# Performance work log

Hardware: AMD Instinct MI355X
Metric: run time of the kernel (lower is better)

## Reference

```python
import jax, jax.numpy as jnp
import numpy as np

B, C, H, W = 4, 128, 64, 64


def setup_inputs() -> dict:
    key = jax.random.key(0)
    ks = jax.random.split(key, 7)
    s = 1.0 / np.sqrt(C)
    return {
        "x": jax.random.normal(ks[0], (B, C, H, W), dtype=jnp.float32),
        "Wq": jax.random.normal(ks[1], (C, C), dtype=jnp.float32) * s,
        "bq": jnp.zeros((C,), dtype=jnp.float32),
        "Wk": jax.random.normal(ks[2], (C, C), dtype=jnp.float32) * s,
        "bk": jnp.zeros((C,), dtype=jnp.float32),
        "Wv": jax.random.normal(ks[3], (C, C), dtype=jnp.float32) * s,
        "bv": jnp.zeros((C,), dtype=jnp.float32),
    }


def reference(x, Wq, bq, Wk, bk, Wv, bv):
    b, c, h, w = x.shape
    n = h * w
    scale = c ** (-0.5)
    # tokens: [B, N, C]
    xt = x.reshape(b, c, n).transpose(0, 2, 1)
    # 1x1 convs == per-token channel GEMMs (out[c'] = sum_c W[c',c] x[c] + b[c'])
    q = jnp.einsum("bnc,dc->bnd", xt, Wq) + bq  # [B, N, C]
    k = jnp.einsum("bnc,dc->bnd", xt, Wk) + bk  # [B, N, C]
    v = jnp.einsum("bnc,dc->bnd", xt, Wv) + bv  # [B, N, C]
    scores = jnp.einsum("bic,bjc->bij", q, k) * scale  # [B, N, N]
    attn = jax.nn.softmax(scores, axis=-1)
    out = jnp.einsum("bij,bjc->bic", attn, v)  # [B, N, C]
    return out.transpose(0, 2, 1).reshape(b, c, h, w)
```

## Files before the change

kernel.cpp:

```cpp
#include <hip/hip_runtime.h>
#include <hip/hip_bf16.h>


#define BATCH 4
#define CH    128
#define NTOK  4096
#define SCALE 0.08838834764831845f
#define LOG2E 1.4426950408889634f
#define MFIX  16.0f

typedef __attribute__((ext_vector_type(8)))  short short8;
typedef __attribute__((ext_vector_type(4)))  float f32x4;
typedef __attribute__((ext_vector_type(16))) float f32x16;

static __device__ __forceinline__ unsigned short f2bf(float f) {
    __hip_bfloat16 h = (__hip_bfloat16)f;
    return *(const unsigned short*)&h;
}

static __device__ __forceinline__ unsigned cvt_pk_bf16(float lo, float hi) {
    unsigned r;
    asm("v_cvt_pk_bf16_f32 %0, %1, %2" : "=v"(r) : "v"(lo), "v"(hi));
    return r;
}

static __device__ __forceinline__ short8 pack_bf16x8(float4 a, float4 b) {
    union { unsigned u[4]; short8 s8; } f;
    f.u[0] = cvt_pk_bf16(a.x, a.y);
    f.u[1] = cvt_pk_bf16(a.z, a.w);
    f.u[2] = cvt_pk_bf16(b.x, b.y);
    f.u[3] = cvt_pk_bf16(b.z, b.w);
    return f.s8;
}

__global__ __launch_bounds__(256) void proj_mfma_kernel(
    const float* __restrict__ x,
    const float* __restrict__ Wq, const float* __restrict__ Wk,
    const float* __restrict__ Wv,
    const float* __restrict__ bq, const float* __restrict__ bk,
    const float* __restrict__ bv,
    unsigned short* __restrict__ q_ws, unsigned short* __restrict__ kf_ws,
    unsigned short* __restrict__ vf_ws)
{
    __shared__ __align__(16) unsigned short Wl[CH * CH];
    __shared__ __align__(16) unsigned short XsT[64 * CH];

    const int t    = threadIdx.x;
    const int w    = t >> 6;
    const int lane = t & 63;
    const int quad = lane >> 4;
    const int c16  = lane & 15;
    const int n0   = blockIdx.x * 64;
    const int b    = blockIdx.y;
    const int z    = blockIdx.z;
    const float* xb = x + (size_t)b * CH * NTOK;
    const float* wm = (z == 0) ? Wq : (z == 1) ? Wk : Wv;

    #pragma unroll
    for (int i = 0; i < 8; ++i) {
        const int f   = i * 256 + t;
        const int row = f >> 4;
        const int u   = f & 15;
        const float* src = wm + f * 8;
        const float4 a = *(const float4*)src;
        const float4 c = *(const float4*)(src + 4);
        *(short8*)&Wl[row * CH + ((u ^ (row & 15)) << 3)] = pack_bf16x8(a, c);
    }
    {
        const int tok = lane;
        #pragma unroll
        for (int cc = 0; cc < 4; ++cc) {
            const int cb = 32 * w + 8 * cc;
            float xv[8];
            #pragma unroll
            for (int j = 0; j < 8; ++j)
                xv[j] = xb[(size_t)(cb + j) * NTOK + n0 + tok];
            union { unsigned u[4]; short8 s8; } pk;
            #pragma unroll
            for (int j = 0; j < 4; ++j)
                pk.u[j] = cvt_pk_bf16(xv[2 * j], xv[2 * j + 1]);
            const int phys = ((cb >> 3) ^ (tok & 15));
            *(short8*)&XsT[tok * CH + phys * 8] = pk.s8;
        }
    }
    __syncthreads();

    if (z < 2) {
        const float* bias = (z == 0) ? bq : bk;
        const float mul = (z == 0) ? (SCALE * LOG2E) : 1.0f;
        short8 xa[4];
        #pragma unroll
        for (int ks = 0; ks < 4; ++ks)
            xa[ks] = *(const short8*)&XsT[(16 * w + c16) * CH + (((4 * ks + quad) ^ c16) << 3)];
        #pragma unroll
        for (int nt = 0; nt < 8; ++nt) {
            f32x4 a = (f32x4){0.f, 0.f, 0.f, 0.f};
            #pragma unroll
            for (int ks = 0; ks < 4; ++ks) {
                const short8 bf = *(const short8*)
                    &Wl[(16 * nt + c16) * CH + (((4 * ks + quad) ^ c16) << 3)];
                a = __builtin_amdgcn_mfma_f32_16x16x32_bf16(xa[ks], bf, a, 0, 0, 0);
            }
            const float bvv = bias[16 * nt + c16];
            #pragma unroll
            for (int r = 0; r < 4; ++r) {
                const int n = n0 + 16 * w + quad * 4 + r;
                if (z == 0) {
                    q_ws[((size_t)b * NTOK + n) * CH + 16 * nt + c16] =
                        f2bf((a[r] + bvv) * mul);
                } else {
                    const size_t idx =
                        (((size_t)b * (NTOK >> 5) + (n >> 5)) * 8 + nt) * 512
                        + ((n & 31) + 32 * (c16 >> 3)) * 8 + (c16 & 7);
                    kf_ws[idx] = f2bf(a[r] + bvv);
                }
            }
        }
    } else {
        #pragma unroll
        for (int nt = 0; nt < 4; ++nt) {
            short8 xbf[4];
            #pragma unroll
            for (int ks = 0; ks < 4; ++ks)
                xbf[ks] = *(const short8*)&XsT[(16 * nt + c16) * CH + (((4 * ks + quad) ^ c16) << 3)];
            #pragma unroll
            for (int mt = 0; mt < 2; ++mt) {
                const int crow16 = 16 * (2 * w + mt);
                f32x4 acc = (f32x4){0.f, 0.f, 0.f, 0.f};
                #pragma unroll
                for (int ks = 0; ks < 4; ++ks) {
                    const short8 wva = *(const short8*)
                        &Wl[(crow16 + c16) * CH + (((4 * ks + quad) ^ c16) << 3)];
                    acc = __builtin_amdgcn_mfma_f32_16x16x32_bf16(wva, xbf[ks], acc, 0, 0, 0);
                }
                #pragma unroll
                for (int r = 0; r < 4; ++r) {
                    const int ch  = crow16 + quad * 4 + r;
                    const int tok = n0 + 16 * nt + c16;
                    const size_t idx =
                        ((((size_t)b * (NTOK >> 5) + (tok >> 5)) * 2
                          + ((tok >> 4) & 1)) * 4 + (ch >> 5)) * 512
                        + ((ch & 31) + 32 * ((tok >> 3) & 1)) * 8 + (tok & 7);
                    vf_ws[idx] = f2bf(acc[r] + bv[ch]);
                }
            }
        }
    }
}

template <int SPLIT>
__global__ __launch_bounds__(256, 2) void flash_attn_mfma(
    const unsigned short* __restrict__ q_ws,
    const unsigned short* __restrict__ kf_ws,
    const unsigned short* __restrict__ vf_ws,
    float* __restrict__ out,
    float* __restrict__ Op, float* __restrict__ l_p)
{
    const int t    = threadIdx.x;
    const int w    = t >> 6;
    const int lane = t & 63;
    const int half = lane >> 5;
    const int l32  = lane & 31;

    int xx, jc, b;
    if constexpr (SPLIT % 2 == 0) {
        const int bid = blockIdx.x;
        b = (bid & 7) >> 1;
        const int sub = (bid & 1) * (16 * SPLIT) + (bid >> 3);
        jc = sub >> 5;
        xx = sub & 31;
    } else {
        const int bid = blockIdx.x;
        xx = bid & 31;
        jc = 0;
        b  = bid >> 5;
    }

    const int n0   = xx * 128;
    const int jbeg = jc * (NTOK / SPLIT);
    constexpr int NT2 = (NTOK / SPLIT) / 32;

    const unsigned short* kg = kf_ws + (size_t)b * NTOK * CH;
    const unsigned short* vg = vf_ws + (size_t)b * NTOK * CH;

    short8 qa[8];
    {
        const unsigned short* qrow =
            q_ws + ((size_t)b * NTOK + n0 + 32 * w + l32) * CH;
        #pragma unroll
        for (int ks = 0; ks < 8; ++ks)
            qa[ks] = *(const short8*)(qrow + ks * 16 + half * 8);
    }

    f32x16 Oa[4];
    #pragma unroll
    for (int ct = 0; ct < 4; ++ct) Oa[ct] = (f32x16)(0.0f);
    float lsum = 0.f;

    short8 kf[8];
    auto KF_LOAD = [&](int jj) {
        const unsigned short* kb = kg + (size_t)(jj >> 5) * (8 * 512);
        #pragma unroll
        for (int ks = 0; ks < 8; ++ks)
            kf[ks] = *(const short8*)(kb + (ks * 64 + lane) * 8);
    };

    KF_LOAD(jbeg);

    for (int i = 0; i < w; ++i) __builtin_amdgcn_s_sleep(4);

    int j0 = jbeg;
    for (int tt = 0; tt < NT2; ++tt, j0 += 32) {
        f32x16 s = (f32x16)(-MFIX);
        __builtin_amdgcn_s_setprio(1);
        #pragma unroll
        for (int ks = 0; ks < 8; ++ks)
            s = __builtin_amdgcn_mfma_f32_32x32x16_bf16(kf[ks], qa[ks], s, 0, 0, 0);
        __builtin_amdgcn_s_setprio(0);

        short8 vfA[4], vfB[4];
        {
            const unsigned short* vb = vg + (size_t)(j0 >> 5) * (8 * 512);
            #pragma unroll
            for (int ct = 0; ct < 4; ++ct)
                vfA[ct] = *(const short8*)(vb + ((0 * 4 + ct) * 64 + lane) * 8);
            #pragma unroll
            for (int ct = 0; ct < 4; ++ct)
                vfB[ct] = *(const short8*)(vb + ((1 * 4 + ct) * 64 + lane) * 8);
        }
        if (tt + 1 < NT2) KF_LOAD(j0 + 32);

        float p[16];
        #pragma unroll
        for (int r = 0; r < 16; ++r) p[r] = exp2f(s[r]);
        {
            float a0 = 0.f, a1 = 0.f, a2 = 0.f, a3 = 0.f;
            #pragma unroll
            for (int r = 0; r < 4; ++r) {
                a0 += p[r]; a1 += p[4 + r]; a2 += p[8 + r]; a3 += p[12 + r];
            }
            lsum += (a0 + a1) + (a2 + a3);
        }
        short8 pb0, pb1;
        {
            unsigned wd[8];
            #pragma unroll
            for (int i = 0; i < 8; ++i) wd[i] = cvt_pk_bf16(p[2 * i], p[2 * i + 1]);
            auto r02 = __builtin_amdgcn_permlane32_swap(wd[0], wd[2], false, false);
            auto r13 = __builtin_amdgcn_permlane32_swap(wd[1], wd[3], false, false);
            auto r46 = __builtin_amdgcn_permlane32_swap(wd[4], wd[6], false, false);
            auto r57 = __builtin_amdgcn_permlane32_swap(wd[5], wd[7], false, false);
            union { unsigned u[4]; short8 s8; } f0, f1;
            f0.u[0] = r02[0]; f0.u[1] = r13[0]; f0.u[2] = r02[1]; f0.u[3] = r13[1];
            f1.u[0] = r46[0]; f1.u[1] = r57[0]; f1.u[2] = r46[1]; f1.u[3] = r57[1];
            pb0 = f0.s8;
            pb1 = f1.s8;
        }

        __builtin_amdgcn_s_setprio(1);
        #pragma unroll
        for (int ct = 0; ct < 4; ++ct)
            Oa[ct] = __builtin_amdgcn_mfma_f32_32x32x16_bf16(vfA[ct], pb0, Oa[ct], 0, 0, 0);
        #pragma unroll
        for (int ct = 0; ct < 4; ++ct)
            Oa[ct] = __builtin_amdgcn_mfma_f32_32x32x16_bf16(vfB[ct], pb1, Oa[ct], 0, 0, 0);
        __builtin_amdgcn_s_setprio(0);
    }

    const float lt = lsum + __shfl_xor(lsum, 32);
    const int n = n0 + 32 * w + l32;

    if constexpr (SPLIT == 1) {
        const float inv = 1.0f / lt;
        #pragma unroll
        for (int ct = 0; ct < 4; ++ct) {
            #pragma unroll
            for (int r = 0; r < 16; ++r) {
                const int c = 32 * ct + (r & 3) + 8 * (r >> 2) + 4 * half;
                out[((size_t)b * CH + c) * NTOK + n] = Oa[ct][r] * inv;
            }
        }
    } else {
        const size_t chunk = (size_t)(b * SPLIT + jc);
        #pragma unroll
        for (int ct = 0; ct < 4; ++ct) {
            #pragma unroll
            for (int r = 0; r < 16; ++r) {
                const int c = 32 * ct + (r & 3) + 8 * (r >> 2) + 4 * half;
                Op[(chunk * CH + c) * NTOK + n] = Oa[ct][r];
            }
        }
        if (half == 0) l_p[chunk * NTOK + n] = lt;
    }
}

template <int SPLIT>
__global__ __launch_bounds__(256) void combine_kernel(
    const float* __restrict__ Op, const float* __restrict__ l_p,
    float* __restrict__ out)
{
    const int b = blockIdx.y;
    const size_t idx = ((size_t)blockIdx.x * 256 + threadIdx.x) * 4;
    const int c = (int)(idx >> 12);
    const int n = (int)(idx & (NTOK - 1));
    float4 acc = make_float4(0.f, 0.f, 0.f, 0.f);
    float4 den = make_float4(0.f, 0.f, 0.f, 0.f);
    #pragma unroll
    for (int j = 0; j < SPLIT; ++j) {
        const size_t chunk = (size_t)(b * SPLIT + j);
        const float4 o = *(const float4*)&Op[(chunk * CH + c) * NTOK + n];
        const float4 d = *(const float4*)&l_p[chunk * NTOK + n];
        acc.x += o.x; acc.y += o.y; acc.z += o.z; acc.w += o.w;
        den.x += d.x; den.y += d.y; den.z += d.z; den.w += d.w;
    }
    float4 r;
    r.x = acc.x / den.x; r.y = acc.y / den.y;
    r.z = acc.z / den.z; r.w = acc.w / den.w;
    *(float4*)&out[((size_t)b * CH * NTOK) + idx] = r;
}

extern "C" void kernel_launch(void* const* d_in, const int* in_sizes, int n_in,
                              void* d_out, int out_size, void* d_ws, size_t ws_size,
                              hipStream_t stream) {
    const float* x  = (const float*)d_in[0];
    const float* Wq = (const float*)d_in[1];
    const float* bq = (const float*)d_in[2];
    const float* Wk = (const float*)d_in[3];
    const float* bk = (const float*)d_in[4];
    const float* Wv = (const float*)d_in[5];
    const float* bv = (const float*)d_in[6];
    float* out = (float*)d_out;

    const size_t QKV = (size_t)BATCH * NTOK * CH;
    unsigned short* q_ws  = (unsigned short*)d_ws;
    unsigned short* kf_ws = q_ws + QKV;
    unsigned short* vf_ws = kf_ws + QKV;
    float* Op = (float*)(vf_ws + QKV);

    const size_t baseBytes = 3 * QKV * 2;
    auto needBytes = [&](size_t S) {
        return baseBytes + S * BATCH * NTOK * (size_t)(CH * 4 + 4);
    };

    dim3 gp(NTOK / 64, BATCH, 3);
    proj_mfma_kernel<<<gp, 256, 0, stream>>>(x, Wq, Wk, Wv, bq, bk, bv,
                                             q_ws, kf_ws, vf_ws);

    dim3 gc(CH * NTOK / 1024, BATCH);
    if (ws_size >= needBytes(4)) {
        float* l_p = Op + (size_t)4 * BATCH * NTOK * CH;
        flash_attn_mfma<4><<<dim3(128 * 4), 256, 0, stream>>>(
            q_ws, kf_ws, vf_ws, out, Op, l_p);
        combine_kernel<4><<<gc, 256, 0, stream>>>(Op, l_p, out);
    } else {
        flash_attn_mfma<1><<<dim3(32 * BATCH), 256, 0, stream>>>(
            q_ws, kf_ws, vf_ws, out, nullptr, nullptr);
    }
}
```

Before: 127.2 us.

## Software-pipeline attention loop: overlap next tile's QK^T with current softmax

Restructures the attention inner loop so QK^T for tile t+1 is issued while the softmax of tile t is computed, with K and V loads prefetched one tile ahead. The aim is to hide exp and permute latency behind MFMA work and to keep the matrix unit busy. It also removes the per-wave s_sleep stagger and the s_setprio priority hints. In exchange it holds two score accumulators live at once, which raises register pressure and could lower occupancy.

```diff
diff --git a/kernel.cpp b/kernel.cpp
--- a/kernel.cpp
+++ b/kernel.cpp
@@ -179,6 +179,7 @@
     const int n0   = xx * 128;
     const int jbeg = jc * (NTOK / SPLIT);
     constexpr int NT2 = (NTOK / SPLIT) / 32;
+    static_assert(NT2 >= 2, "pipeline needs >= 2 tiles");
 
     const unsigned short* kg = kf_ws + (size_t)b * NTOK * CH;
     const unsigned short* vg = vf_ws + (size_t)b * NTOK * CH;
@@ -198,73 +199,82 @@
     float lsum = 0.f;
 
     short8 kf[8];
+    short8 vfA[4], vfB[4];
+
     auto KF_LOAD = [&](int jj) {
         const unsigned short* kb = kg + (size_t)(jj >> 5) * (8 * 512);
         #pragma unroll
         for (int ks = 0; ks < 8; ++ks)
             kf[ks] = *(const short8*)(kb + (ks * 64 + lane) * 8);
     };
-
-    KF_LOAD(jbeg);
-
-    for (int i = 0; i < w; ++i) __builtin_amdgcn_s_sleep(4);
-
-    int j0 = jbeg;
-    for (int tt = 0; tt < NT2; ++tt, j0 += 32) {
-        f32x16 s = (f32x16)(-MFIX);
-        __builtin_amdgcn_s_setprio(1);
+    auto VF_LOAD = [&](int jj) {
+        const unsigned short* vb = vg + (size_t)(jj >> 5) * (8 * 512);
+        #pragma unroll
+        for (int ct = 0; ct < 4; ++ct)
+            vfA[ct] = *(const short8*)(vb + ((0 * 4 + ct) * 64 + lane) * 8);
+        #pragma unroll
+        for (int ct = 0; ct < 4; ++ct)
+            vfB[ct] = *(const short8*)(vb + ((1 * 4 + ct) * 64 + lane) * 8);
+    };
+    auto QKT = [&](f32x16& s) {
         #pragma unroll
         for (int ks = 0; ks < 8; ++ks)
             s = __builtin_amdgcn_mfma_f32_32x32x16_bf16(kf[ks], qa[ks], s, 0, 0, 0);
-        __builtin_amdgcn_s_setprio(0);
-
-        short8 vfA[4], vfB[4];
-        {
-            const unsigned short* vb = vg + (size_t)(j0 >> 5) * (8 * 512);
-            #pragma unroll
-            for (int ct = 0; ct < 4; ++ct)
-                vfA[ct] = *(const short8*)(vb + ((0 * 4 + ct) * 64 + lane) * 8);
-            #pragma unroll
-            for (int ct = 0; ct < 4; ++ct)
-                vfB[ct] = *(const short8*)(vb + ((1 * 4 + ct) * 64 + lane) * 8);
-        }
-        if (tt + 1 < NT2) KF_LOAD(j0 + 32);
-
+    };
+    auto SOFTMAX = [&](const f32x16& s, short8& pb0, short8& pb1) {
         float p[16];
         #pragma unroll
         for (int r = 0; r < 16; ++r) p[r] = exp2f(s[r]);
-        {
-            float a0 = 0.f, a1 = 0.f, a2 = 0.f, a3 = 0.f;
-            #pragma unroll
-            for (int r = 0; r < 4; ++r) {
-                a0 += p[r]; a1 += p[4 + r]; a2 += p[8 + r]; a3 += p[12 + r];
-            }
-            lsum += (a0 + a1) + (a2 + a3);
-        }
-        short8 pb0, pb1;
-        {
-            unsigned wd[8];
-            #pragma unroll
-            for (int i = 0; i < 8; ++i) wd[i] = cvt_pk_bf16(p[2 * i], p[2 * i + 1]);
-            auto r02 = __builtin_amdgcn_permlane32_swap(wd[0], wd[2], false, false);
-            auto r13 = __builtin_amdgcn_permlane32_swap(wd[1], wd[3], false, false);
-            auto r46 = __builtin_amdgcn_permlane32_swap(wd[4], wd[6], false, false);
-            auto r57 = __builtin_amdgcn_permlane32_swap(wd[5], wd[7], false, false);
-            union { unsigned u[4]; short8 s8; } f0, f1;
-            f0.u[0] = r02[0]; f0.u[1] = r13[0]; f0.u[2] = r02[1]; f0.u[3] = r13[1];
-            f1.u[0] = r46[0]; f1.u[1] = r57[0]; f1.u[2] = r46[1]; f1.u[3] = r57[1];
-            pb0 = f0.s8;
-            pb1 = f1.s8;
-        }
-
-        __builtin_amdgcn_s_setprio(1);
+        float a0 = 0.f, a1 = 0.f, a2 = 0.f, a3 = 0.f;
+        #pragma unroll
+        for (int r = 0; r < 4; ++r) {
+            a0 += p[r]; a1 += p[4 + r]; a2 += p[8 + r]; a3 += p[12 + r];
+        }
+        lsum += (a0 + a1) + (a2 + a3);
+        unsigned wd[8];
+        #pragma unroll
+        for (int i = 0; i < 8; ++i) wd[i] = cvt_pk_bf16(p[2 * i], p[2 * i + 1]);
+        auto r02 = __builtin_amdgcn_permlane32_swap(wd[0], wd[2], false, false);
+        auto r13 = __builtin_amdgcn_permlane32_swap(wd[1], wd[3], false, false);
+        auto r46 = __builtin_amdgcn_permlane32_swap(wd[4], wd[6], false, false);
+        auto r57 = __builtin_amdgcn_permlane32_swap(wd[5], wd[7], false, false);
+        union { unsigned u[4]; short8 s8; } f0, f1;
+        f0.u[0] = r02[0]; f0.u[1] = r13[0]; f0.u[2] = r02[1]; f0.u[3] = r13[1];
+        f1.u[0] = r46[0]; f1.u[1] = r57[0]; f1.u[2] = r46[1]; f1.u[3] = r57[1];
+        pb0 = f0.s8;
+        pb1 = f1.s8;
+    };
+    auto PV = [&](const short8& pb0, const short8& pb1) {
         #pragma unroll
         for (int ct = 0; ct < 4; ++ct)
             Oa[ct] = __builtin_amdgcn_mfma_f32_32x32x16_bf16(vfA[ct], pb0, Oa[ct], 0, 0, 0);
         #pragma unroll
         for (int ct = 0; ct < 4; ++ct)
             Oa[ct] = __builtin_amdgcn_mfma_f32_32x32x16_bf16(vfB[ct], pb1, Oa[ct], 0, 0, 0);
-        __builtin_amdgcn_s_setprio(0);
+    };
+
+    KF_LOAD(jbeg);
+    f32x16 sX = (f32x16)(-MFIX);
+    QKT(sX);
+    KF_LOAD(jbeg + 32);
+    VF_LOAD(jbeg);
+
+    int j0 = jbeg;
+    for (int tt = 0; tt + 1 < NT2; ++tt, j0 += 32) {
+        short8 pb0, pb1;
+        f32x16 sY = (f32x16)(-MFIX);
+        SOFTMAX(sX, pb0, pb1);
+        QKT(sY);
+        if (tt + 2 < NT2) KF_LOAD(j0 + 64);
+        PV(pb0, pb1);
+        VF_LOAD(j0 + 32);
+        sX = sY;
+    }
+
+    {
+        short8 pb0, pb1;
+        SOFTMAX(sX, pb0, pb1);
+        PV(pb0, pb1);
     }
 
     const float lt = lsum + __shfl_xor(lsum, 32);
```

Result: slower. 226.8 us (+78.3%).
